# Optimization experiments

Hardware: AMD Instinct MI355X
Metric: run time of the kernel (lower is better)

Reference implementation:

```python
import jax, jax.numpy as jnp
import numpy as np

NQ = 4
PI_HALF = np.pi / 2
HAD = jnp.array([[1, 1], [1, -1]], dtype=jnp.complex64) / np.sqrt(2)
CNOT = jnp.array([[1, 0, 0, 0], [0, 1, 0, 0], [0, 0, 0, 1], [0, 0, 1, 0]], dtype=jnp.complex64)
_bits = (np.arange(2 ** NQ)[:, None] >> np.arange(NQ - 1, -1, -1)[None, :]) & 1
ZSIGNS = jnp.asarray(1.0 - 2.0 * _bits, jnp.float32)  # [16, NQ]


def _ry(theta):
    c = jnp.cos(theta / 2).astype(jnp.complex64)
    s = jnp.sin(theta / 2).astype(jnp.complex64)
    return jnp.stack([jnp.stack([c, -s], -1), jnp.stack([s, c], -1)], -2)  # [...,2,2]


def _rot(phi, theta, omega):
    # PennyLane Rot = RZ(omega) @ RY(theta) @ RZ(phi)
    c = jnp.cos(theta / 2).astype(jnp.complex64)
    s = jnp.sin(theta / 2).astype(jnp.complex64)
    ep = jnp.exp(0.5j * phi).astype(jnp.complex64)
    eo = jnp.exp(0.5j * omega).astype(jnp.complex64)
    return jnp.stack([jnp.stack([jnp.conj(ep) * jnp.conj(eo) * c, -ep * jnp.conj(eo) * s]),
                      jnp.stack([jnp.conj(ep) * eo * s, ep * eo * c])])


def _cry(theta):
    # controlled-RY, batched: [B] -> [B,4,4], basis order (control, target)
    B = theta.shape[0]
    U = jnp.zeros((B, 4, 4), jnp.complex64).at[:, 0, 0].set(1.0).at[:, 1, 1].set(1.0)
    return U.at[:, 2:, 2:].set(_ry(theta))


def _apply1(state, U, wire):
    s = jnp.moveaxis(state, wire + 1, 1)
    shp = s.shape
    s = s.reshape(shp[0], 2, -1)
    s = jnp.einsum('ij,bjk->bik', U, s) if U.ndim == 2 else jnp.einsum('bij,bjk->bik', U, s)
    return jnp.moveaxis(s.reshape(shp), 1, wire + 1)


def _apply2(state, U, q0, q1):
    s = jnp.moveaxis(state, (q0 + 1, q1 + 1), (1, 2))
    shp = s.shape
    s = s.reshape(shp[0], 4, -1)
    s = jnp.einsum('ij,bjk->bik', U, s) if U.ndim == 2 else jnp.einsum('bij,bjk->bik', U, s)
    return jnp.moveaxis(s.reshape(shp), (1, 2), (q0 + 1, q1 + 1))


def _init_state(B):
    s = jnp.zeros((B, 2 ** NQ), jnp.complex64).at[:, 0].set(1.0)
    return s.reshape((B,) + (2,) * NQ)


def _zexp(state):
    p = state.reshape(state.shape[0], -1)
    p = p.real ** 2 + p.imag ** 2
    return p @ ZSIGNS  # [B, NQ]


def _attention_circuit(q, k, params):
    # q, k: [E, NQ] angles; params: [NQ, 3] shared
    s = _init_state(q.shape[0])
    for i in range(NQ):
        s = _apply1(s, _ry(q[:, i]), i)
    for i in range(NQ):
        s = _apply1(s, HAD, i)
    for i in range(NQ):
        s = _apply2(s, _cry(k[:, i]), i, (i + 1) % NQ)
    for i in range(NQ):
        s = _apply1(s, _rot(params[i, 0], params[i, 1], params[i, 2]), i)
    return _zexp(s)


def _entangle_circuit(x, params):
    # x: [N, NQ] angles; params: [n_layers, NQ, 3]
    s = _init_state(x.shape[0])
    for i in range(NQ):
        s = _apply1(s, _ry(x[:, i]), i)
    for l in range(params.shape[0]):
        for i in range(NQ - 1):
            s = _apply2(s, CNOT, i, i + 1)
        for i in range(NQ):
            s = _apply1(s, _rot(params[l, i, 0], params[l, i, 1], params[l, i, 2]), i)
        s = _apply2(s, CNOT, 0, NQ - 1)  # n_qubits >= 4
    return _zexp(s)


def _path_circuit(x, params):
    # x: [N, NQ]; params: [3, NQ, 3]
    s = _init_state(x.shape[0])
    for i in range(NQ):
        s = _apply1(s, HAD, i)
    for i in range(NQ):
        s = _apply1(s, _ry(x[:, i]), i)
    for l in range(3):
        for i in range(NQ):
            s = _apply1(s, _rot(params[l, i, 0], params[l, i, 1], params[l, i, 2]), i)
        for i in range(NQ - 1):
            s = _apply2(s, CNOT, i, i + 1)
    return _zexp(s)


def _forward(x, W_in, b_in, lin_W, lin_b, qproj_W, qproj_b, ent_params,
             attq_W, attq_b, attk_W, attk_b, att_qp, path_params,
             path_in_W, path_in_b, path_out_W, path_out_b, out_W, out_b, edge_index):
    N = x.shape[0]
    loops = jnp.arange(N, dtype=edge_index.dtype)
    ei = jnp.concatenate([edge_index, jnp.stack([loops, loops])], axis=1)  # add_self_loops
    src, dst = ei[0], ei[1]
    h = jax.nn.relu(x @ W_in.T + b_in)
    for l in range(lin_W.shape[0]):
        x_cls = h @ lin_W[l].T + lin_b[l]
        xq = _entangle_circuit(jnp.tanh(h[:, :NQ]) * PI_HALF, ent_params[l])
        x_comb = x_cls + xq @ qproj_W[l].T + qproj_b[l]
        q = jnp.tanh(h @ attq_W[l].T + attq_b[l]) * PI_HALF
        k = jnp.tanh(h @ attk_W[l].T + attk_b[l]) * PI_HALF
        scores = _attention_circuit(q[src], k[dst], att_qp[l]).mean(axis=1)  # [E]
        att = jax.nn.softmax(scores)  # global softmax over all edges (faithful)
        h = jax.ops.segment_sum(att[:, None] * x_comb[src], dst, num_segments=N)
        h = jax.nn.relu(h)  # dropout is identity at eval
    pq = jnp.tanh(h @ path_in_W.T + path_in_b) * PI_HALF
    h = _path_circuit(pq, path_params) @ path_out_W.T + path_out_b
    return h @ out_W.T + out_b


def setup_inputs() -> dict:
    key = jax.random.key(0)
    ks = jax.random.split(key, 22)
    N, E, D_in, D_h, D_out, L = 20000, 300000, 64, 128, 32, 2
    w = lambda k, shape: jax.random.normal(k, shape, jnp.float32) * 0.1
    return {
        'x': jax.random.normal(ks[0], (N, D_in), jnp.float32),
        'W_in': w(ks[1], (D_h, D_in)), 'b_in': w(ks[2], (D_h,)),
        'lin_W': w(ks[3], (L, D_h, D_h)), 'lin_b': w(ks[4], (L, D_h)),
        'qproj_W': w(ks[5], (L, D_h, NQ)), 'qproj_b': w(ks[6], (L, D_h)),
        'ent_params': w(ks[7], (L, 2, NQ, 3)),
        'attq_W': w(ks[8], (L, NQ, D_h)), 'attq_b': w(ks[9], (L, NQ)),
        'attk_W': w(ks[10], (L, NQ, D_h)), 'attk_b': w(ks[11], (L, NQ)),
        'att_qp': w(ks[12], (L, NQ, 3)),
        'path_params': w(ks[13], (3, NQ, 3)),
        'path_in_W': w(ks[14], (NQ, D_h)), 'path_in_b': w(ks[15], (NQ,)),
        'path_out_W': w(ks[16], (D_h, NQ)), 'path_out_b': w(ks[17], (D_h,)),
        'out_W': w(ks[18], (D_out, D_h)), 'out_b': w(ks[19], (D_out,)),
        'edge_index': jax.random.randint(ks[20], (2, E), 0, N, dtype=jnp.int32),
    }


def reference(x, W_in, b_in, lin_W, lin_b, qproj_W, qproj_b, ent_params,
              attq_W, attq_b, attk_W, attk_b, att_qp, path_params,
              path_in_W, path_in_b, path_out_W, path_out_b, out_W, out_b, edge_index):
    return _forward(x, W_in, b_in, lin_W, lin_b, qproj_W, qproj_b, ent_params,
                    attq_W, attq_b, attk_W, attk_b, att_qp, path_params,
                    path_in_W, path_in_b, path_out_W, path_out_b, out_W, out_b, edge_index)
```

## Files before the change

### kernel.cpp

```cpp
#include <hip/hip_runtime.h>
#include <math.h>

#define PI_HALF 1.57079632679489662f

__device__ __forceinline__ float fast_tanh(float x) {
    float e = __expf(2.f * x);
    return 1.f - 2.f * __builtin_amdgcn_rcpf(e + 1.f);
}


__device__ __forceinline__ void init_state(float sr[16], float si[16]) {
#pragma unroll
    for (int i = 0; i < 16; ++i) { sr[i] = 0.f; si[i] = 0.f; }
    sr[0] = 1.f;
}

template<int M>
__device__ __forceinline__ void ry_g(float sr[16], float si[16], float c, float s) {
#pragma unroll
    for (int i = 0; i < 16; ++i) {
        if (i & M) continue;
        const int j = i | M;
        float ar = sr[i], ai = si[i], br = sr[j], bi = si[j];
        sr[i] = c * ar - s * br;  si[i] = c * ai - s * bi;
        sr[j] = s * ar + c * br;  si[j] = s * ai + c * bi;
    }
}

template<int M>
__device__ __forceinline__ void had_g(float sr[16], float si[16]) {
    const float r = 0.70710678118654752f;
#pragma unroll
    for (int i = 0; i < 16; ++i) {
        if (i & M) continue;
        const int j = i | M;
        float ar = sr[i], ai = si[i], br = sr[j], bi = si[j];
        sr[i] = (ar + br) * r;  si[i] = (ai + bi) * r;
        sr[j] = (ar - br) * r;  si[j] = (ai - bi) * r;
    }
}

template<int MC, int MT>
__device__ __forceinline__ void cnot_g(float sr[16], float si[16]) {
#pragma unroll
    for (int i = 0; i < 16; ++i) {
        if (!(i & MC) || (i & MT)) continue;
        const int j = i | MT;
        float tr = sr[i], ti = si[i];
        sr[i] = sr[j]; si[i] = si[j];
        sr[j] = tr;    si[j] = ti;
    }
}

template<int MC, int MT>
__device__ __forceinline__ void cry_g(float sr[16], float si[16], float c, float s) {
#pragma unroll
    for (int i = 0; i < 16; ++i) {
        if (!(i & MC) || (i & MT)) continue;
        const int j = i | MT;
        float ar = sr[i], ai = si[i], br = sr[j], bi = si[j];
        sr[i] = c * ar - s * br;  si[i] = c * ai - s * bi;
        sr[j] = s * ar + c * br;  si[j] = s * ai + c * bi;
    }
}

template<int M>
__device__ __forceinline__ void rot_pre(float sr[16], float si[16], const float* __restrict__ u) {
    const float u00r = u[0], u00i = u[1], u01r = u[2], u01i = u[3];
    const float u10r = u[4], u10i = u[5], u11r = u[6], u11i = u[7];
#pragma unroll
    for (int i = 0; i < 16; ++i) {
        if (i & M) continue;
        const int j = i | M;
        float ar = sr[i], ai = si[i], br = sr[j], bi = si[j];
        sr[i] = u00r * ar - u00i * ai + u01r * br - u01i * bi;
        si[i] = u00r * ai + u00i * ar + u01r * bi + u01i * br;
        sr[j] = u10r * ar - u10i * ai + u11r * br - u11i * bi;
        si[j] = u10r * ai + u10i * ar + u11r * bi + u11i * br;
    }
}

__device__ __forceinline__ void zexp_g(const float sr[16], const float si[16], float z[4]) {
    float p[16];
#pragma unroll
    for (int i = 0; i < 16; ++i) p[i] = sr[i] * sr[i] + si[i] * si[i];
    z[0] = z[1] = z[2] = z[3] = 0.f;
#pragma unroll
    for (int i = 0; i < 16; ++i) {
        z[0] += (i & 8) ? -p[i] : p[i];
        z[1] += (i & 4) ? -p[i] : p[i];
        z[2] += (i & 2) ? -p[i] : p[i];
        z[3] += (i & 1) ? -p[i] : p[i];
    }
}

__global__ void k_setup(const float* __restrict__ entp, const float* __restrict__ attqp,
                        const float* __restrict__ pparm,
                        const float* __restrict__ outW, const float* __restrict__ outb,
                        const float* __restrict__ poW, const float* __restrict__ pob,
                        float* __restrict__ rotbuf, float* __restrict__ M,
                        float* __restrict__ v) {
    const int t = threadIdx.x;
    if (t < 36) {
        const float* p;
        if (t < 16)      p = entp  + t * 3;
        else if (t < 24) p = attqp + (t - 16) * 3;
        else             p = pparm + (t - 24) * 3;
        float phi = p[0], theta = p[1], omega = p[2];
        float st, ct; sincosf(0.5f * theta, &st, &ct);
        float sp, cp; sincosf(0.5f * (phi + omega), &sp, &cp);
        float sm, cm; sincosf(0.5f * (phi - omega), &sm, &cm);
        float* u = rotbuf + t * 8;
        u[0] =  ct * cp;  u[1] = -ct * sp;
        u[2] = -st * cm;  u[3] = -st * sm;
        u[4] =  st * cm;  u[5] = -st * sm;
        u[6] =  ct * cp;  u[7] =  ct * sp;
    } else if (t >= 64 && t < 192) {
        int t2 = t - 64;
        int o = t2 >> 2, i = t2 & 3;
        float acc = 0.f;
        for (int j = 0; j < 128; ++j) acc += outW[o * 128 + j] * poW[j * 4 + i];
        M[t2] = acc;
    } else if (t >= 192 && t < 224) {
        int o = t - 192;
        float acc = outb[o];
        for (int j = 0; j < 128; ++j) acc += outW[o * 128 + j] * pob[j];
        v[o] = acc;
    }
}


__global__ void k_in(const float* __restrict__ x, const float* __restrict__ W,
                     const float* __restrict__ b, float* __restrict__ h, int N) {
    __shared__ float xs[16 * 64];
    const int base = blockIdx.x * 16;
    const int tid = threadIdx.x;
    for (int idx = tid; idx < 16 * 64; idx += 128) {
        int n = base + (idx >> 6);
        xs[idx] = (n < N) ? x[(size_t)n * 64 + (idx & 63)] : 0.f;
    }
    __syncthreads();
    float acc[16];
#pragma unroll
    for (int n = 0; n < 16; ++n) acc[n] = 0.f;
    const float4* wr4 = (const float4*)(W + tid * 64);
    for (int c4 = 0; c4 < 16; ++c4) {
        float4 w = wr4[c4];
#pragma unroll
        for (int n = 0; n < 16; ++n) {
            float4 hv = *(const float4*)&xs[n * 64 + c4 * 4];
            acc[n] += w.x * hv.x + w.y * hv.y + w.z * hv.z + w.w * hv.w;
        }
    }
    const float bb = b[tid];
#pragma unroll
    for (int n = 0; n < 16; ++n) {
        int node = base + n;
        if (node < N) h[(size_t)node * 128 + tid] = fmaxf(acc[n] + bb, 0.f);
    }
}

__global__ void k_ent(const float* __restrict__ h, const float* __restrict__ rotE,
                      float* __restrict__ xq, int N) {
    int n = blockIdx.x * blockDim.x + threadIdx.x;
    if (n >= N) return;
    float4 hv = *(const float4*)&h[(size_t)n * 128];
    float sr[16], si[16];
    init_state(sr, si);
    { float s, c; __sincosf(fast_tanh(hv.x) * (0.5f * PI_HALF), &s, &c); ry_g<8>(sr, si, c, s); }
    { float s, c; __sincosf(fast_tanh(hv.y) * (0.5f * PI_HALF), &s, &c); ry_g<4>(sr, si, c, s); }
    { float s, c; __sincosf(fast_tanh(hv.z) * (0.5f * PI_HALF), &s, &c); ry_g<2>(sr, si, c, s); }
    { float s, c; __sincosf(fast_tanh(hv.w) * (0.5f * PI_HALF), &s, &c); ry_g<1>(sr, si, c, s); }
#pragma unroll
    for (int l = 0; l < 2; ++l) {
        cnot_g<8, 4>(sr, si); cnot_g<4, 2>(sr, si); cnot_g<2, 1>(sr, si);
        const float* P = rotE + l * 32;
        rot_pre<8>(sr, si, P);
        rot_pre<4>(sr, si, P + 8);
        rot_pre<2>(sr, si, P + 16);
        rot_pre<1>(sr, si, P + 24);
        cnot_g<8, 1>(sr, si);
    }
    float z[4]; zexp_g(sr, si, z);
    *(float4*)&xq[(size_t)n * 4] = make_float4(z[0], z[1], z[2], z[3]);
}

__global__ void k_lin(const float* __restrict__ h, const float* __restrict__ xq,
                      const float* __restrict__ linW, const float* __restrict__ linb,
                      const float* __restrict__ qpW, const float* __restrict__ qpb,
                      const float* __restrict__ aqW, const float* __restrict__ aqb,
                      const float* __restrict__ akW, const float* __restrict__ akb,
                      float* __restrict__ xcomb, float* __restrict__ qbuf,
                      float* __restrict__ kbuf, int N) {
    __shared__ float hs[16 * 128];
    __shared__ float xqs[16 * 4];
    const int base = blockIdx.x * 16;
    const int tid = threadIdx.x;
    for (int idx = tid; idx < 16 * 128; idx += 128) {
        int n = base + (idx >> 7);
        hs[idx] = (n < N) ? h[(size_t)n * 128 + (idx & 127)] : 0.f;
    }
    if (tid < 64) {
        int n = base + (tid >> 2);
        xqs[tid] = (n < N) ? xq[(size_t)n * 4 + (tid & 3)] : 0.f;
    }
    __syncthreads();
    float acc[16];
#pragma unroll
    for (int n = 0; n < 16; ++n) acc[n] = 0.f;
    const float4* wr4 = (const float4*)(linW + tid * 128);
    for (int c4 = 0; c4 < 32; ++c4) {
        float4 w = wr4[c4];
#pragma unroll
        for (int n = 0; n < 16; ++n) {
            float4 hv = *(const float4*)&hs[n * 128 + c4 * 4];
            acc[n] += w.x * hv.x + w.y * hv.y + w.z * hv.z + w.w * hv.w;
        }
    }
    const float bb = linb[tid] + qpb[tid];
    const float qw0 = qpW[tid * 4 + 0], qw1 = qpW[tid * 4 + 1];
    const float qw2 = qpW[tid * 4 + 2], qw3 = qpW[tid * 4 + 3];
#pragma unroll
    for (int n = 0; n < 16; ++n) {
        int node = base + n;
        if (node < N) {
            xcomb[(size_t)node * 128 + tid] = acc[n] + bb
                + qw0 * xqs[n * 4 + 0] + qw1 * xqs[n * 4 + 1]
                + qw2 * xqs[n * 4 + 2] + qw3 * xqs[n * 4 + 3];
        }
    }
    const int nl = tid >> 3;
    const int which = tid & 7;
    const int qi = which & 3;
    const float4* Wp4 = (const float4*)(((which < 4) ? aqW : akW) + qi * 128);
    float dot = (which < 4) ? aqb[qi] : akb[qi];
    for (int c4 = 0; c4 < 32; ++c4) {
        float4 w = Wp4[c4];
        float4 hv = *(const float4*)&hs[nl * 128 + c4 * 4];
        dot += w.x * hv.x + w.y * hv.y + w.z * hv.z + w.w * hv.w;
    }
    int node = base + nl;
    if (node < N) {
        float half = fast_tanh(dot) * (0.5f * PI_HALF);
        float s, c; __sincosf(half, &s, &c);
        float* dst = ((which < 4) ? qbuf : kbuf) + (size_t)node * 8 + qi * 2;
        dst[0] = c; dst[1] = s;
    }
}

__global__ void k_att(const float* __restrict__ qb, const float* __restrict__ kb,
                      const int* __restrict__ ei, const float* __restrict__ RA,
                      const int* __restrict__ inv, float* __restrict__ escore,
                      float* __restrict__ sumexp, int E, int EP) {
    __shared__ float red[256];
    int e = blockIdx.x * blockDim.x + threadIdx.x;
    float ex = 0.f;
    if (e < EP) {
        int s_, d_;
        if (e < E) { s_ = ei[e]; d_ = ei[E + e]; } else { s_ = d_ = e - E; }
        float4 qa = *(const float4*)&qb[(size_t)s_ * 8];
        float4 qc = *(const float4*)&qb[(size_t)s_ * 8 + 4];
        float4 ka = *(const float4*)&kb[(size_t)d_ * 8];
        float4 kc = *(const float4*)&kb[(size_t)d_ * 8 + 4];
        float sr[16], si[16];
        init_state(sr, si);
        ry_g<8>(sr, si, qa.x, qa.y);
        ry_g<4>(sr, si, qa.z, qa.w);
        ry_g<2>(sr, si, qc.x, qc.y);
        ry_g<1>(sr, si, qc.z, qc.w);
        had_g<8>(sr, si); had_g<4>(sr, si); had_g<2>(sr, si); had_g<1>(sr, si);
        cry_g<8, 4>(sr, si, ka.x, ka.y);
        cry_g<4, 2>(sr, si, ka.z, ka.w);
        cry_g<2, 1>(sr, si, kc.x, kc.y);
        cry_g<1, 8>(sr, si, kc.z, kc.w);
        rot_pre<8>(sr, si, RA);
        rot_pre<4>(sr, si, RA + 8);
        rot_pre<2>(sr, si, RA + 16);
        rot_pre<1>(sr, si, RA + 24);
        float z[4]; zexp_g(sr, si, z);
        float sc = 0.25f * (z[0] + z[1] + z[2] + z[3]);
        ex = __expf(sc);
        escore[inv[e]] = ex;
    }
    red[threadIdx.x] = ex;
    __syncthreads();
    for (int s = 128; s > 0; s >>= 1) {
        if ((int)threadIdx.x < s) red[threadIdx.x] += red[threadIdx.x + s];
        __syncthreads();
    }
    if (threadIdx.x == 0) atomicAdd(sumexp, red[0]);
}


__global__ void k_hist(const int* __restrict__ ei, int* __restrict__ cnt, int E, int EP) {
    int e = blockIdx.x * blockDim.x + threadIdx.x;
    if (e >= EP) return;
    int d_ = (e < E) ? ei[E + e] : e - E;
    atomicAdd(&cnt[d_], 1);
}

__global__ void k_scan(const int* __restrict__ cnt, int* __restrict__ off,
                       int* __restrict__ cur, int N) {
    __shared__ int tot[1024];
    const int t = threadIdx.x;
    const int chunk = (N + 1023) >> 10;
    const int s0 = t * chunk;
    const int s1 = min(s0 + chunk, N);
    int sum = 0;
    for (int i = s0; i < s1; ++i) sum += cnt[i];
    tot[t] = sum;
    __syncthreads();
    for (int d = 1; d < 1024; d <<= 1) {
        int v = (t >= d) ? tot[t - d] : 0;
        __syncthreads();
        tot[t] += v;
        __syncthreads();
    }
    int run = (t == 0) ? 0 : tot[t - 1];
    for (int i = s0; i < s1; ++i) {
        off[i] = run; cur[i] = run;
        run += cnt[i];
    }
}

__global__ void k_fill(const int* __restrict__ ei, int* __restrict__ cur,
                       int* __restrict__ srcs, int* __restrict__ inv, int E, int EP) {
    int e = blockIdx.x * blockDim.x + threadIdx.x;
    if (e >= EP) return;
    int s_, d_;
    if (e < E) { s_ = ei[e]; d_ = ei[E + e]; } else { s_ = d_ = e - E; }
    int pos = atomicAdd(&cur[d_], 1);
    srcs[pos] = s_;
    inv[e] = pos;
}

__global__ void k_gather(const float* __restrict__ xcomb, const int* __restrict__ srcs,
                         const float* __restrict__ escore, const int* __restrict__ off,
                         const int* __restrict__ cnt, const float* __restrict__ sumexp,
                         float* __restrict__ h) {
    __shared__ int sS[128];
    __shared__ float wS[128];
    const int b = blockIdx.x;
    const int tid = threadIdx.x;
    const int start = off[b];
    const int num = cnt[b];
    float acc = 0.f;
    for (int base = 0; base < num; base += 128) {
        int m = min(128, num - base);
        if (tid < m) {
            sS[tid] = srcs[start + base + tid];
            wS[tid] = escore[start + base + tid];
        }
        __syncthreads();
        for (int i = 0; i < m; ++i)
            acc += wS[i] * xcomb[(size_t)sS[i] * 128 + tid];
        __syncthreads();
    }
    const float invS = __builtin_amdgcn_rcpf(sumexp[0]);
    h[(size_t)b * 128 + tid] = fmaxf(acc * invS, 0.f);
}

#define PQ_STRIDE 132
__global__ void k_pq(const float* __restrict__ h, const float* __restrict__ piW,
                     const float* __restrict__ pib, float* __restrict__ pq8, int N) {
    __shared__ float hs[32 * PQ_STRIDE];
    const int base = blockIdx.x * 32;
    const int tid = threadIdx.x;
    for (int idx = tid; idx < 32 * 128; idx += 128) {
        int n = base + (idx >> 7);
        hs[(idx >> 7) * PQ_STRIDE + (idx & 127)] = (n < N) ? h[(size_t)n * 128 + (idx & 127)] : 0.f;
    }
    __syncthreads();
    const int nl = tid >> 2;
    const int i  = tid & 3;
    float dot = pib[i];
    const float4* w4 = (const float4*)(piW + i * 128);
    for (int c4 = 0; c4 < 32; ++c4) {
        float4 w = w4[c4];
        float4 hv = *(const float4*)&hs[nl * PQ_STRIDE + c4 * 4];
        dot += w.x * hv.x + w.y * hv.y + w.z * hv.z + w.w * hv.w;
    }
    int node = base + nl;
    if (node < N) {
        float half = fast_tanh(dot) * (0.5f * PI_HALF);
        float s, c; __sincosf(half, &s, &c);
        pq8[(size_t)node * 8 + i * 2]     = c;
        pq8[(size_t)node * 8 + i * 2 + 1] = s;
    }
}

__global__ void k_pathc(const float* __restrict__ pq8, const float* __restrict__ RP,
                        const float* __restrict__ M, const float* __restrict__ v,
                        float* __restrict__ out, int N) {
    __shared__ float zS[256 * 4];
    __shared__ float MS[128];
    __shared__ float vS[32];
    const int tid = threadIdx.x;
    if (tid < 128) MS[tid] = M[tid];
    else if (tid < 160) vS[tid - 128] = v[tid - 128];
    __syncthreads();
    const int base = blockIdx.x * 256;
    const int n = base + tid;
    if (n < N) {
        float4 pa = *(const float4*)&pq8[(size_t)n * 8];
        float4 pc = *(const float4*)&pq8[(size_t)n * 8 + 4];
        float sr[16], si[16];
        init_state(sr, si);
        had_g<8>(sr, si); had_g<4>(sr, si); had_g<2>(sr, si); had_g<1>(sr, si);
        ry_g<8>(sr, si, pa.x, pa.y);
        ry_g<4>(sr, si, pa.z, pa.w);
        ry_g<2>(sr, si, pc.x, pc.y);
        ry_g<1>(sr, si, pc.z, pc.w);
#pragma unroll
        for (int l = 0; l < 3; ++l) {
            const float* P = RP + l * 32;
            rot_pre<8>(sr, si, P);
            rot_pre<4>(sr, si, P + 8);
            rot_pre<2>(sr, si, P + 16);
            rot_pre<1>(sr, si, P + 24);
            cnot_g<8, 4>(sr, si); cnot_g<4, 2>(sr, si); cnot_g<2, 1>(sr, si);
        }
        float z[4]; zexp_g(sr, si, z);
        zS[tid * 4 + 0] = z[0]; zS[tid * 4 + 1] = z[1];
        zS[tid * 4 + 2] = z[2]; zS[tid * 4 + 3] = z[3];
    }
    __syncthreads();
#pragma unroll
    for (int k = 0; k < 32; ++k) {
        int flat = k * 256 + tid;
        int nl = flat >> 5;
        int o = flat & 31;
        int node = base + nl;
        if (node < N) {
            out[(size_t)node * 32 + o] = vS[o]
                + MS[o * 4 + 0] * zS[nl * 4 + 0] + MS[o * 4 + 1] * zS[nl * 4 + 1]
                + MS[o * 4 + 2] * zS[nl * 4 + 2] + MS[o * 4 + 3] * zS[nl * 4 + 3];
        }
    }
}


extern "C" void kernel_launch(void* const* d_in, const int* in_sizes, int n_in,
                              void* d_out, int out_size, void* d_ws, size_t ws_size,
                              hipStream_t stream) {
    const float* x     = (const float*)d_in[0];
    const float* W_in  = (const float*)d_in[1];
    const float* b_in  = (const float*)d_in[2];
    const float* linW  = (const float*)d_in[3];
    const float* linb  = (const float*)d_in[4];
    const float* qpW   = (const float*)d_in[5];
    const float* qpb   = (const float*)d_in[6];
    const float* entp  = (const float*)d_in[7];
    const float* aqW   = (const float*)d_in[8];
    const float* aqb   = (const float*)d_in[9];
    const float* akW   = (const float*)d_in[10];
    const float* akb   = (const float*)d_in[11];
    const float* attqp = (const float*)d_in[12];
    const float* pparm = (const float*)d_in[13];
    const float* piW   = (const float*)d_in[14];
    const float* pib   = (const float*)d_in[15];
    const float* poW   = (const float*)d_in[16];
    const float* pob   = (const float*)d_in[17];
    const float* outW  = (const float*)d_in[18];
    const float* outb  = (const float*)d_in[19];
    const int*   ei    = (const int*)d_in[20];

    const int N  = in_sizes[0] / 64;
    const int E  = in_sizes[20] / 2;
    const int EP = E + N;

    float* ws     = (float*)d_ws;
    float* h      = ws;
    float* xcomb  = h      + (size_t)N * 128;
    float* xq     = xcomb  + (size_t)N * 128;
    float* qbuf   = xq     + (size_t)N * 4;
    float* kbuf   = qbuf   + (size_t)N * 8;
    float* pq8    = kbuf   + (size_t)N * 8;
    float* escore = pq8    + (size_t)N * 8;
    float* rotbuf = escore + EP;
    float* Mm     = rotbuf + 36 * 8;
    float* vv     = Mm + 128;
    int*   cnt    = (int*)(vv + 32);
    float* sumexp = (float*)(cnt + N);
    int*   off    = (int*)(sumexp + 4);
    int*   cur    = off + N;
    int*   srcs   = cur + N;
    int*   inv    = srcs + EP;

    const float* rotE = rotbuf;
    const float* rotA = rotbuf + 128;
    const float* rotP = rotbuf + 192;

    const int nb16 = (N + 15) / 16;
    const int ebl  = (EP + 255) / 256;

    hipMemsetAsync(cnt, 0, (size_t)(N + 4) * sizeof(int), stream);
    k_hist<<<ebl, 256, 0, stream>>>(ei, cnt, E, EP);
    k_scan<<<1, 1024, 0, stream>>>(cnt, off, cur, N);
    k_fill<<<ebl, 256, 0, stream>>>(ei, cur, srcs, inv, E, EP);
    k_setup<<<1, 256, 0, stream>>>(entp, attqp, pparm, outW, outb, poW, pob,
                                   rotbuf, Mm, vv);
    k_in<<<nb16, 128, 0, stream>>>(x, W_in, b_in, h, N);

    for (int l = 0; l < 2; ++l) {
        k_ent<<<(N + 255) / 256, 256, 0, stream>>>(h, rotE + l * 64, xq, N);
        k_lin<<<nb16, 128, 0, stream>>>(h, xq,
            linW + (size_t)l * 128 * 128, linb + l * 128,
            qpW + (size_t)l * 128 * 4, qpb + l * 128,
            aqW + (size_t)l * 4 * 128, aqb + l * 4,
            akW + (size_t)l * 4 * 128, akb + l * 4,
            xcomb, qbuf, kbuf, N);
        k_att<<<ebl, 256, 0, stream>>>(qbuf, kbuf, ei, rotA + l * 32, inv,
                                       escore, sumexp + l, E, EP);
        k_gather<<<N, 128, 0, stream>>>(xcomb, srcs, escore, off, cnt, sumexp + l, h);
    }

    k_pq<<<(N + 31) / 32, 128, 0, stream>>>(h, piW, pib, pq8, N);
    k_pathc<<<(N + 255) / 256, 256, 0, stream>>>(pq8, rotP, Mm, vv, (float*)d_out, N);
}
```

Measured before the change: 397.0 us.

## Fuse entanglement into linear kernel, fuse path kernels, iterate attention in CSR order

The entanglement circuit now runs inside the linear kernel on 16 extra threads, and the path projection and path circuit are merged into one kernel. This removes launches and the xq and pq8 round trips through global memory. Attention now walks edges in destination-sorted order using srcs/dsts arrays instead of an inverse permutation, and its block reduction uses wavefront shuffles. The linear and input GEMMs use 256-thread blocks with padded shared-memory rows to avoid bank conflicts. The risks are serialized circuit work on only 16 or 64 threads per block, and less parallelism in the path kernel.

```diff
diff --git a/kernel.cpp b/kernel.cpp
--- a/kernel.cpp
+++ b/kernel.cpp
@@ -130,134 +130,183 @@
 }
 
 
-__global__ void k_in(const float* __restrict__ x, const float* __restrict__ W,
-                     const float* __restrict__ b, float* __restrict__ h, int N) {
-    __shared__ float xs[16 * 64];
+__global__ void k_hist(const int* __restrict__ ei, int* __restrict__ cnt, int E, int EP) {
+    int e = blockIdx.x * blockDim.x + threadIdx.x;
+    if (e >= EP) return;
+    int d_ = (e < E) ? ei[E + e] : e - E;
+    atomicAdd(&cnt[d_], 1);
+}
+
+__global__ void k_scan(const int* __restrict__ cnt, int* __restrict__ off,
+                       int* __restrict__ cur, int N) {
+    __shared__ int tot[1024];
+    const int t = threadIdx.x;
+    const int chunk = (N + 1023) >> 10;
+    const int s0 = t * chunk;
+    const int s1 = min(s0 + chunk, N);
+    int sum = 0;
+    for (int i = s0; i < s1; ++i) sum += cnt[i];
+    tot[t] = sum;
+    __syncthreads();
+    for (int d = 1; d < 1024; d <<= 1) {
+        int v = (t >= d) ? tot[t - d] : 0;
+        __syncthreads();
+        tot[t] += v;
+        __syncthreads();
+    }
+    int run = (t == 0) ? 0 : tot[t - 1];
+    for (int i = s0; i < s1; ++i) {
+        off[i] = run; cur[i] = run;
+        run += cnt[i];
+    }
+}
+
+__global__ void k_fill(const int* __restrict__ ei, int* __restrict__ cur,
+                       int* __restrict__ srcs, int* __restrict__ dsts, int E, int EP) {
+    int e = blockIdx.x * blockDim.x + threadIdx.x;
+    if (e >= EP) return;
+    int s_, d_;
+    if (e < E) { s_ = ei[e]; d_ = ei[E + e]; } else { s_ = d_ = e - E; }
+    int pos = atomicAdd(&cur[d_], 1);
+    srcs[pos] = s_;
+    dsts[pos] = d_;
+}
+
+
+#define XS 68
+__global__ __launch_bounds__(256) void k_in(
+        const float* __restrict__ x, const float* __restrict__ W,
+        const float* __restrict__ b, float* __restrict__ h, int N) {
+    __shared__ float xs[16 * XS];
     const int base = blockIdx.x * 16;
     const int tid = threadIdx.x;
-    for (int idx = tid; idx < 16 * 64; idx += 128) {
+    for (int idx = tid; idx < 16 * 64; idx += 256) {
         int n = base + (idx >> 6);
-        xs[idx] = (n < N) ? x[(size_t)n * 64 + (idx & 63)] : 0.f;
-    }
-    __syncthreads();
-    float acc[16];
-#pragma unroll
-    for (int n = 0; n < 16; ++n) acc[n] = 0.f;
-    const float4* wr4 = (const float4*)(W + tid * 64);
+        xs[(idx >> 6) * XS + (idx & 63)] = (n < N) ? x[(size_t)n * 64 + (idx & 63)] : 0.f;
+    }
+    __syncthreads();
+    const int o  = tid & 127;
+    const int nh = tid >> 7;
+    float acc[8];
+#pragma unroll
+    for (int i = 0; i < 8; ++i) acc[i] = 0.f;
+    const float4* w4 = (const float4*)(W + o * 64);
     for (int c4 = 0; c4 < 16; ++c4) {
-        float4 w = wr4[c4];
-#pragma unroll
-        for (int n = 0; n < 16; ++n) {
-            float4 hv = *(const float4*)&xs[n * 64 + c4 * 4];
-            acc[n] += w.x * hv.x + w.y * hv.y + w.z * hv.z + w.w * hv.w;
-        }
-    }
-    const float bb = b[tid];
-#pragma unroll
-    for (int n = 0; n < 16; ++n) {
-        int node = base + n;
-        if (node < N) h[(size_t)node * 128 + tid] = fmaxf(acc[n] + bb, 0.f);
-    }
-}
-
-__global__ void k_ent(const float* __restrict__ h, const float* __restrict__ rotE,
-                      float* __restrict__ xq, int N) {
-    int n = blockIdx.x * blockDim.x + threadIdx.x;
-    if (n >= N) return;
-    float4 hv = *(const float4*)&h[(size_t)n * 128];
-    float sr[16], si[16];
-    init_state(sr, si);
-    { float s, c; __sincosf(fast_tanh(hv.x) * (0.5f * PI_HALF), &s, &c); ry_g<8>(sr, si, c, s); }
-    { float s, c; __sincosf(fast_tanh(hv.y) * (0.5f * PI_HALF), &s, &c); ry_g<4>(sr, si, c, s); }
-    { float s, c; __sincosf(fast_tanh(hv.z) * (0.5f * PI_HALF), &s, &c); ry_g<2>(sr, si, c, s); }
-    { float s, c; __sincosf(fast_tanh(hv.w) * (0.5f * PI_HALF), &s, &c); ry_g<1>(sr, si, c, s); }
-#pragma unroll
-    for (int l = 0; l < 2; ++l) {
-        cnot_g<8, 4>(sr, si); cnot_g<4, 2>(sr, si); cnot_g<2, 1>(sr, si);
-        const float* P = rotE + l * 32;
-        rot_pre<8>(sr, si, P);
-        rot_pre<4>(sr, si, P + 8);
-        rot_pre<2>(sr, si, P + 16);
-        rot_pre<1>(sr, si, P + 24);
-        cnot_g<8, 1>(sr, si);
-    }
-    float z[4]; zexp_g(sr, si, z);
-    *(float4*)&xq[(size_t)n * 4] = make_float4(z[0], z[1], z[2], z[3]);
-}
-
-__global__ void k_lin(const float* __restrict__ h, const float* __restrict__ xq,
-                      const float* __restrict__ linW, const float* __restrict__ linb,
-                      const float* __restrict__ qpW, const float* __restrict__ qpb,
-                      const float* __restrict__ aqW, const float* __restrict__ aqb,
-                      const float* __restrict__ akW, const float* __restrict__ akb,
-                      float* __restrict__ xcomb, float* __restrict__ qbuf,
-                      float* __restrict__ kbuf, int N) {
-    __shared__ float hs[16 * 128];
-    __shared__ float xqs[16 * 4];
+        float4 w = w4[c4];
+#pragma unroll
+        for (int i = 0; i < 8; ++i) {
+            float4 hv = *(const float4*)&xs[(nh * 8 + i) * XS + c4 * 4];
+            acc[i] += w.x * hv.x + w.y * hv.y + w.z * hv.z + w.w * hv.w;
+        }
+    }
+    const float bb = b[o];
+#pragma unroll
+    for (int i = 0; i < 8; ++i) {
+        int node = base + nh * 8 + i;
+        if (node < N) h[(size_t)node * 128 + o] = fmaxf(acc[i] + bb, 0.f);
+    }
+}
+
+#define HS 132
+__global__ __launch_bounds__(256) void k_lin(
+        const float* __restrict__ h,
+        const float* __restrict__ linW, const float* __restrict__ linb,
+        const float* __restrict__ qpW, const float* __restrict__ qpb,
+        const float* __restrict__ aqW, const float* __restrict__ aqb,
+        const float* __restrict__ akW, const float* __restrict__ akb,
+        const float* __restrict__ rotE,
+        float* __restrict__ xcomb, float* __restrict__ qbuf,
+        float* __restrict__ kbuf, int N) {
+    __shared__ float hs[16 * HS];
+    __shared__ float zS[16 * 4];
     const int base = blockIdx.x * 16;
     const int tid = threadIdx.x;
-    for (int idx = tid; idx < 16 * 128; idx += 128) {
+    for (int idx = tid; idx < 16 * 128; idx += 256) {
         int n = base + (idx >> 7);
-        hs[idx] = (n < N) ? h[(size_t)n * 128 + (idx & 127)] : 0.f;
-    }
-    if (tid < 64) {
-        int n = base + (tid >> 2);
-        xqs[tid] = (n < N) ? xq[(size_t)n * 4 + (tid & 3)] : 0.f;
-    }
-    __syncthreads();
-    float acc[16];
-#pragma unroll
-    for (int n = 0; n < 16; ++n) acc[n] = 0.f;
-    const float4* wr4 = (const float4*)(linW + tid * 128);
+        hs[(idx >> 7) * HS + (idx & 127)] = (n < N) ? h[(size_t)n * 128 + (idx & 127)] : 0.f;
+    }
+    __syncthreads();
+
+    const int o  = tid & 127;
+    const int nh = tid >> 7;
+    float acc[8];
+#pragma unroll
+    for (int i = 0; i < 8; ++i) acc[i] = 0.f;
+    const float4* w4 = (const float4*)(linW + o * 128);
     for (int c4 = 0; c4 < 32; ++c4) {
-        float4 w = wr4[c4];
-#pragma unroll
-        for (int n = 0; n < 16; ++n) {
-            float4 hv = *(const float4*)&hs[n * 128 + c4 * 4];
-            acc[n] += w.x * hv.x + w.y * hv.y + w.z * hv.z + w.w * hv.w;
-        }
-    }
-    const float bb = linb[tid] + qpb[tid];
-    const float qw0 = qpW[tid * 4 + 0], qw1 = qpW[tid * 4 + 1];
-    const float qw2 = qpW[tid * 4 + 2], qw3 = qpW[tid * 4 + 3];
-#pragma unroll
-    for (int n = 0; n < 16; ++n) {
-        int node = base + n;
+        float4 w = w4[c4];
+#pragma unroll
+        for (int i = 0; i < 8; ++i) {
+            float4 hv = *(const float4*)&hs[(nh * 8 + i) * HS + c4 * 4];
+            acc[i] += w.x * hv.x + w.y * hv.y + w.z * hv.z + w.w * hv.w;
+        }
+    }
+
+    if (tid < 128) {
+        const int nl = tid >> 3;
+        const int which = tid & 7;
+        const int qi = which & 3;
+        const float4* Wp4 = (const float4*)(((which < 4) ? aqW : akW) + qi * 128);
+        float dot = (which < 4) ? aqb[qi] : akb[qi];
+        for (int c4 = 0; c4 < 32; ++c4) {
+            float4 w = Wp4[c4];
+            float4 hv = *(const float4*)&hs[nl * HS + c4 * 4];
+            dot += w.x * hv.x + w.y * hv.y + w.z * hv.z + w.w * hv.w;
+        }
+        int node = base + nl;
         if (node < N) {
-            xcomb[(size_t)node * 128 + tid] = acc[n] + bb
-                + qw0 * xqs[n * 4 + 0] + qw1 * xqs[n * 4 + 1]
-                + qw2 * xqs[n * 4 + 2] + qw3 * xqs[n * 4 + 3];
-        }
-    }
-    const int nl = tid >> 3;
-    const int which = tid & 7;
-    const int qi = which & 3;
-    const float4* Wp4 = (const float4*)(((which < 4) ? aqW : akW) + qi * 128);
-    float dot = (which < 4) ? aqb[qi] : akb[qi];
-    for (int c4 = 0; c4 < 32; ++c4) {
-        float4 w = Wp4[c4];
-        float4 hv = *(const float4*)&hs[nl * 128 + c4 * 4];
-        dot += w.x * hv.x + w.y * hv.y + w.z * hv.z + w.w * hv.w;
-    }
-    int node = base + nl;
-    if (node < N) {
-        float half = fast_tanh(dot) * (0.5f * PI_HALF);
-        float s, c; __sincosf(half, &s, &c);
-        float* dst = ((which < 4) ? qbuf : kbuf) + (size_t)node * 8 + qi * 2;
-        dst[0] = c; dst[1] = s;
+            float half = fast_tanh(dot) * (0.5f * PI_HALF);
+            float s, c; __sincosf(half, &s, &c);
+            float* dst = ((which < 4) ? qbuf : kbuf) + (size_t)node * 8 + qi * 2;
+            dst[0] = c; dst[1] = s;
+        }
+    } else if (tid < 144) {
+        const int en = tid - 128;
+        float4 hv = *(const float4*)&hs[en * HS];
+        float sr[16], si[16];
+        init_state(sr, si);
+        { float s, c; __sincosf(fast_tanh(hv.x) * (0.5f * PI_HALF), &s, &c); ry_g<8>(sr, si, c, s); }
+        { float s, c; __sincosf(fast_tanh(hv.y) * (0.5f * PI_HALF), &s, &c); ry_g<4>(sr, si, c, s); }
+        { float s, c; __sincosf(fast_tanh(hv.z) * (0.5f * PI_HALF), &s, &c); ry_g<2>(sr, si, c, s); }
+        { float s, c; __sincosf(fast_tanh(hv.w) * (0.5f * PI_HALF), &s, &c); ry_g<1>(sr, si, c, s); }
+#pragma unroll
+        for (int l = 0; l < 2; ++l) {
+            cnot_g<8, 4>(sr, si); cnot_g<4, 2>(sr, si); cnot_g<2, 1>(sr, si);
+            const float* P = rotE + l * 32;
+            rot_pre<8>(sr, si, P);
+            rot_pre<4>(sr, si, P + 8);
+            rot_pre<2>(sr, si, P + 16);
+            rot_pre<1>(sr, si, P + 24);
+            cnot_g<8, 1>(sr, si);
+        }
+        float z[4]; zexp_g(sr, si, z);
+        zS[en * 4 + 0] = z[0]; zS[en * 4 + 1] = z[1];
+        zS[en * 4 + 2] = z[2]; zS[en * 4 + 3] = z[3];
+    }
+    __syncthreads();
+
+    const float bb = linb[o] + qpb[o];
+    const float4 qw = *(const float4*)(qpW + o * 4);
+#pragma unroll
+    for (int i = 0; i < 8; ++i) {
+        int node = base + nh * 8 + i;
+        if (node < N) {
+            float4 z = *(const float4*)&zS[(nh * 8 + i) * 4];
+            xcomb[(size_t)node * 128 + o] = acc[i] + bb
+                + qw.x * z.x + qw.y * z.y + qw.z * z.z + qw.w * z.w;
+        }
     }
 }
 
 __global__ void k_att(const float* __restrict__ qb, const float* __restrict__ kb,
-                      const int* __restrict__ ei, const float* __restrict__ RA,
-                      const int* __restrict__ inv, float* __restrict__ escore,
-                      float* __restrict__ sumexp, int E, int EP) {
-    __shared__ float red[256];
-    int e = blockIdx.x * blockDim.x + threadIdx.x;
+                      const int* __restrict__ srcs, const int* __restrict__ dsts,
+                      const float* __restrict__ RA, float* __restrict__ escore,
+                      float* __restrict__ sumexp, int EP) {
+    __shared__ float red[4];
+    int p = blockIdx.x * blockDim.x + threadIdx.x;
     float ex = 0.f;
-    if (e < EP) {
-        int s_, d_;
-        if (e < E) { s_ = ei[e]; d_ = ei[E + e]; } else { s_ = d_ = e - E; }
+    if (p < EP) {
+        int s_ = srcs[p], d_ = dsts[p];
         float4 qa = *(const float4*)&qb[(size_t)s_ * 8];
         float4 qc = *(const float4*)&qb[(size_t)s_ * 8 + 4];
         float4 ka = *(const float4*)&kb[(size_t)d_ * 8];
@@ -280,58 +329,15 @@
         float z[4]; zexp_g(sr, si, z);
         float sc = 0.25f * (z[0] + z[1] + z[2] + z[3]);
         ex = __expf(sc);
-        escore[inv[e]] = ex;
-    }
-    red[threadIdx.x] = ex;
-    __syncthreads();
-    for (int s = 128; s > 0; s >>= 1) {
-        if ((int)threadIdx.x < s) red[threadIdx.x] += red[threadIdx.x + s];
-        __syncthreads();
-    }
-    if (threadIdx.x == 0) atomicAdd(sumexp, red[0]);
-}
-
-
-__global__ void k_hist(const int* __restrict__ ei, int* __restrict__ cnt, int E, int EP) {
-    int e = blockIdx.x * blockDim.x + threadIdx.x;
-    if (e >= EP) return;
-    int d_ = (e < E) ? ei[E + e] : e - E;
-    atomicAdd(&cnt[d_], 1);
-}
-
-__global__ void k_scan(const int* __restrict__ cnt, int* __restrict__ off,
-                       int* __restrict__ cur, int N) {
-    __shared__ int tot[1024];
-    const int t = threadIdx.x;
-    const int chunk = (N + 1023) >> 10;
-    const int s0 = t * chunk;
-    const int s1 = min(s0 + chunk, N);
-    int sum = 0;
-    for (int i = s0; i < s1; ++i) sum += cnt[i];
-    tot[t] = sum;
-    __syncthreads();
-    for (int d = 1; d < 1024; d <<= 1) {
-        int v = (t >= d) ? tot[t - d] : 0;
-        __syncthreads();
-        tot[t] += v;
-        __syncthreads();
-    }
-    int run = (t == 0) ? 0 : tot[t - 1];
-    for (int i = s0; i < s1; ++i) {
-        off[i] = run; cur[i] = run;
-        run += cnt[i];
-    }
-}
-
-__global__ void k_fill(const int* __restrict__ ei, int* __restrict__ cur,
-                       int* __restrict__ srcs, int* __restrict__ inv, int E, int EP) {
-    int e = blockIdx.x * blockDim.x + threadIdx.x;
-    if (e >= EP) return;
-    int s_, d_;
-    if (e < E) { s_ = ei[e]; d_ = ei[E + e]; } else { s_ = d_ = e - E; }
-    int pos = atomicAdd(&cur[d_], 1);
-    srcs[pos] = s_;
-    inv[e] = pos;
+        escore[p] = ex;
+    }
+    float w = ex;
+#pragma unroll
+    for (int d = 32; d > 0; d >>= 1) w += __shfl_down(w, d, 64);
+    if ((threadIdx.x & 63) == 0) red[threadIdx.x >> 6] = w;
+    __syncthreads();
+    if (threadIdx.x == 0)
+        atomicAdd(sumexp, red[0] + red[1] + red[2] + red[3]);
 }
 
 __global__ void k_gather(const float* __restrict__ xcomb, const int* __restrict__ srcs,
@@ -360,57 +366,50 @@
     h[(size_t)b * 128 + tid] = fmaxf(acc * invS, 0.f);
 }
 
-#define PQ_STRIDE 132
-__global__ void k_pq(const float* __restrict__ h, const float* __restrict__ piW,
-                     const float* __restrict__ pib, float* __restrict__ pq8, int N) {
-    __shared__ float hs[32 * PQ_STRIDE];
-    const int base = blockIdx.x * 32;
-    const int tid = threadIdx.x;
-    for (int idx = tid; idx < 32 * 128; idx += 128) {
-        int n = base + (idx >> 7);
-        hs[(idx >> 7) * PQ_STRIDE + (idx & 127)] = (n < N) ? h[(size_t)n * 128 + (idx & 127)] : 0.f;
-    }
-    __syncthreads();
-    const int nl = tid >> 2;
-    const int i  = tid & 3;
-    float dot = pib[i];
-    const float4* w4 = (const float4*)(piW + i * 128);
-    for (int c4 = 0; c4 < 32; ++c4) {
-        float4 w = w4[c4];
-        float4 hv = *(const float4*)&hs[nl * PQ_STRIDE + c4 * 4];
-        dot += w.x * hv.x + w.y * hv.y + w.z * hv.z + w.w * hv.w;
-    }
-    int node = base + nl;
-    if (node < N) {
-        float half = fast_tanh(dot) * (0.5f * PI_HALF);
-        float s, c; __sincosf(half, &s, &c);
-        pq8[(size_t)node * 8 + i * 2]     = c;
-        pq8[(size_t)node * 8 + i * 2 + 1] = s;
-    }
-}
-
-__global__ void k_pathc(const float* __restrict__ pq8, const float* __restrict__ RP,
-                        const float* __restrict__ M, const float* __restrict__ v,
-                        float* __restrict__ out, int N) {
-    __shared__ float zS[256 * 4];
+__global__ __launch_bounds__(256) void k_path(
+        const float* __restrict__ h, const float* __restrict__ piW,
+        const float* __restrict__ pib, const float* __restrict__ RP,
+        const float* __restrict__ M, const float* __restrict__ v,
+        float* __restrict__ out, int N) {
+    __shared__ float hs[64 * HS];
+    __shared__ float pqS[64 * 9];
+    __shared__ float zS[64 * 4];
     __shared__ float MS[128];
     __shared__ float vS[32];
+    const int base = blockIdx.x * 64;
     const int tid = threadIdx.x;
     if (tid < 128) MS[tid] = M[tid];
     else if (tid < 160) vS[tid - 128] = v[tid - 128];
-    __syncthreads();
-    const int base = blockIdx.x * 256;
-    const int n = base + tid;
-    if (n < N) {
-        float4 pa = *(const float4*)&pq8[(size_t)n * 8];
-        float4 pc = *(const float4*)&pq8[(size_t)n * 8 + 4];
+    for (int idx = tid; idx < 64 * 128; idx += 256) {
+        int n = base + (idx >> 7);
+        hs[(idx >> 7) * HS + (idx & 127)] = (n < N) ? h[(size_t)n * 128 + (idx & 127)] : 0.f;
+    }
+    __syncthreads();
+    {
+        const int nl = tid >> 2;
+        const int i  = tid & 3;
+        float dot = pib[i];
+        const float4* w4 = (const float4*)(piW + i * 128);
+        for (int c4 = 0; c4 < 32; ++c4) {
+            float4 w = w4[c4];
+            float4 hv = *(const float4*)&hs[nl * HS + c4 * 4];
+            dot += w.x * hv.x + w.y * hv.y + w.z * hv.z + w.w * hv.w;
+        }
+        float half = fast_tanh(dot) * (0.5f * PI_HALF);
+        float s, c; __sincosf(half, &s, &c);
+        pqS[nl * 9 + i * 2]     = c;
+        pqS[nl * 9 + i * 2 + 1] = s;
+    }
+    __syncthreads();
+    if (tid < 64) {
+        const float* p = pqS + tid * 9;
         float sr[16], si[16];
         init_state(sr, si);
         had_g<8>(sr, si); had_g<4>(sr, si); had_g<2>(sr, si); had_g<1>(sr, si);
-        ry_g<8>(sr, si, pa.x, pa.y);
-        ry_g<4>(sr, si, pa.z, pa.w);
-        ry_g<2>(sr, si, pc.x, pc.y);
-        ry_g<1>(sr, si, pc.z, pc.w);
+        ry_g<8>(sr, si, p[0], p[1]);
+        ry_g<4>(sr, si, p[2], p[3]);
+        ry_g<2>(sr, si, p[4], p[5]);
+        ry_g<1>(sr, si, p[6], p[7]);
 #pragma unroll
         for (int l = 0; l < 3; ++l) {
             const float* P = RP + l * 32;
@@ -426,7 +425,7 @@
     }
     __syncthreads();
 #pragma unroll
-    for (int k = 0; k < 32; ++k) {
+    for (int k = 0; k < 8; ++k) {
         int flat = k * 256 + tid;
         int nl = flat >> 5;
         int o = flat & 31;
@@ -472,11 +471,9 @@
     float* ws     = (float*)d_ws;
     float* h      = ws;
     float* xcomb  = h      + (size_t)N * 128;
-    float* xq     = xcomb  + (size_t)N * 128;
-    float* qbuf   = xq     + (size_t)N * 4;
+    float* qbuf   = xcomb  + (size_t)N * 128;
     float* kbuf   = qbuf   + (size_t)N * 8;
-    float* pq8    = kbuf   + (size_t)N * 8;
-    float* escore = pq8    + (size_t)N * 8;
+    float* escore = kbuf   + (size_t)N * 8;
     float* rotbuf = escore + EP;
     float* Mm     = rotbuf + 36 * 8;
     float* vv     = Mm + 128;
@@ -485,7 +482,7 @@
     int*   off    = (int*)(sumexp + 4);
     int*   cur    = off + N;
     int*   srcs   = cur + N;
-    int*   inv    = srcs + EP;
+    int*   dsts   = srcs + EP;
 
     const float* rotE = rotbuf;
     const float* rotA = rotbuf + 128;
@@ -497,24 +494,23 @@
     hipMemsetAsync(cnt, 0, (size_t)(N + 4) * sizeof(int), stream);
     k_hist<<<ebl, 256, 0, stream>>>(ei, cnt, E, EP);
     k_scan<<<1, 1024, 0, stream>>>(cnt, off, cur, N);
-    k_fill<<<ebl, 256, 0, stream>>>(ei, cur, srcs, inv, E, EP);
+    k_fill<<<ebl, 256, 0, stream>>>(ei, cur, srcs, dsts, E, EP);
     k_setup<<<1, 256, 0, stream>>>(entp, attqp, pparm, outW, outb, poW, pob,
                                    rotbuf, Mm, vv);
-    k_in<<<nb16, 128, 0, stream>>>(x, W_in, b_in, h, N);
+    k_in<<<nb16, 256, 0, stream>>>(x, W_in, b_in, h, N);
 
     for (int l = 0; l < 2; ++l) {
-        k_ent<<<(N + 255) / 256, 256, 0, stream>>>(h, rotE + l * 64, xq, N);
-        k_lin<<<nb16, 128, 0, stream>>>(h, xq,
+        k_lin<<<nb16, 256, 0, stream>>>(h,
             linW + (size_t)l * 128 * 128, linb + l * 128,
             qpW + (size_t)l * 128 * 4, qpb + l * 128,
             aqW + (size_t)l * 4 * 128, aqb + l * 4,
             akW + (size_t)l * 4 * 128, akb + l * 4,
-            xcomb, qbuf, kbuf, N);
-        k_att<<<ebl, 256, 0, stream>>>(qbuf, kbuf, ei, rotA + l * 32, inv,
-                                       escore, sumexp + l, E, EP);
+            rotE + l * 64, xcomb, qbuf, kbuf, N);
+        k_att<<<ebl, 256, 0, stream>>>(qbuf, kbuf, srcs, dsts, rotA + l * 32,
+                                       escore, sumexp + l, EP);
         k_gather<<<N, 128, 0, stream>>>(xcomb, srcs, escore, off, cnt, sumexp + l, h);
     }
 
-    k_pq<<<(N + 31) / 32, 128, 0, stream>>>(h, piW, pib, pq8, N);
-    k_pathc<<<(N + 255) / 256, 256, 0, stream>>>(pq8, rotP, Mm, vv, (float*)d_out, N);
-}
+    k_path<<<(N + 63) / 64, 256, 0, stream>>>(h, piW, pib, rotP, Mm, vv,
+                                              (float*)d_out, N);
+}
```

New measurement: 415.5 us. +4.7%, slower.
